# Optimization experiments

Hardware: AMD Instinct MI355X
Metric: run time of the kernel (lower is better)

## Reference

```python
import jax, jax.numpy as jnp
import numpy as np

B, N, IN_DIM = 2, 2048, 1024
DIM, DEPTH, HEADS, DH = 512, 4, 8, 128
INNER = HEADS * DH  # 1024
MLP, NCLS = 1024, 2
EPS = 1e-5


def setup_inputs() -> dict:
    key = jax.random.key(0)
    ks = jax.random.split(key, 10)
    r = lambda k, shape: (jax.random.normal(k, shape, dtype=jnp.float32) * 0.02)
    return {
        "x": jax.random.normal(ks[0], (B, N, IN_DIM), dtype=jnp.float32),
        "mask": jnp.ones((B, N), dtype=jnp.float32),
        "proj_w": r(ks[1], (IN_DIM, DIM)),
        "proj_b": jnp.zeros((DIM,), jnp.float32),
        "cls_token": jax.random.normal(ks[2], (1, 1, DIM), dtype=jnp.float32),
        "ln1_g": jnp.ones((DEPTH, DIM), jnp.float32),
        "ln1_b": jnp.zeros((DEPTH, DIM), jnp.float32),
        "qkv_w": r(ks[3], (DEPTH, DIM, 3 * INNER)),
        "out_w": r(ks[4], (DEPTH, INNER, DIM)),
        "out_b": jnp.zeros((DEPTH, DIM), jnp.float32),
        "ln2_g": jnp.ones((DEPTH, DIM), jnp.float32),
        "ln2_b": jnp.zeros((DEPTH, DIM), jnp.float32),
        "ff_w1": r(ks[5], (DEPTH, DIM, MLP)),
        "ff_b1": jnp.zeros((DEPTH, MLP), jnp.float32),
        "ff_w2": r(ks[6], (DEPTH, MLP, DIM)),
        "ff_b2": jnp.zeros((DEPTH, DIM), jnp.float32),
        "norm_g": jnp.ones((DIM,), jnp.float32),
        "norm_b": jnp.zeros((DIM,), jnp.float32),
        "head_ln_g": jnp.ones((DIM,), jnp.float32),
        "head_ln_b": jnp.zeros((DIM,), jnp.float32),
        "head_w": r(ks[7], (DIM, NCLS)),
        "head_b": jnp.zeros((NCLS,), jnp.float32),
    }


def _ln(x, g, b):
    m = jnp.mean(x, axis=-1, keepdims=True)
    v = jnp.mean((x - m) ** 2, axis=-1, keepdims=True)
    return (x - m) * jax.lax.rsqrt(v + EPS) * g + b


def reference(x, mask, proj_w, proj_b, cls_token, ln1_g, ln1_b, qkv_w, out_w,
              out_b, ln2_g, ln2_b, ff_w1, ff_b1, ff_w2, ff_b2, norm_g, norm_b,
              head_ln_g, head_ln_b, head_w, head_b):
    b = x.shape[0]
    scale = DH ** -0.5
    # input projection + ReLU
    h = jax.nn.relu(x @ proj_w + proj_b)  # [b, n, dim]
    # prepend cls token; extend mask with a 1 for it
    cls = jnp.broadcast_to(cls_token, (b, 1, DIM))
    h = jnp.concatenate([cls, h], axis=1)  # [b, n+1, dim]
    m_full = jnp.concatenate([jnp.ones((b, 1), mask.dtype), mask], axis=1)
    keep = (m_full != 0)[:, None, None, :]  # [b,1,1,n+1]

    for l in range(DEPTH):  # NOTE: original blocks have NO residual connections
        hn = _ln(h, ln1_g[l], ln1_b[l])
        qkv = hn @ qkv_w[l]  # [b, n+1, 3*inner]
        q, k, v = jnp.split(qkv, 3, axis=-1)
        resh = lambda t: t.reshape(b, -1, HEADS, DH).transpose(0, 2, 1, 3)
        q, k, v = resh(q), resh(k), resh(v)  # [b, h, n+1, dh]
        dots = jnp.einsum('bhid,bhjd->bhij', q, k) * scale
        dots = jnp.where(keep, dots, -jnp.inf)
        attn = jax.nn.softmax(dots, axis=-1)
        o = jnp.einsum('bhij,bhjd->bhid', attn, v)
        o = o.transpose(0, 2, 1, 3).reshape(b, -1, INNER)
        h = o @ out_w[l] + out_b[l]  # attention out (no residual)
        hn = _ln(h, ln2_g[l], ln2_b[l])
        h = jax.nn.gelu(hn @ ff_w1[l] + ff_b1[l], approximate=False) @ ff_w2[l] + ff_b2[l]

    pooled = h[:, 0]  # cls pooling
    pooled = _ln(pooled, norm_g, norm_b)
    pooled = _ln(pooled, head_ln_g, head_ln_b)
    return pooled @ head_w + head_b  # [b, num_classes]
```

## Files before the change

kernel.cpp:

```cpp
#include <hip/hip_runtime.h>
#include <hip/hip_bf16.h>
#include <stdint.h>

#define B_      2
#define N_      2048
#define S_      2049
#define SP_     2176
#define MP_     (B_*SP_)
#define IN_DIM_ 1024
#define DIM_    512
#define HEADS_  8
#define DH_     128
#define INNER_  1024
#define MLP_    1024
#define DEPTH_  4
#define NKV_    (SP_/64)
#define NCHUNK_ 3
#define TPC_    12

typedef __bf16 bf16;
typedef __bf16 bf16x4 __attribute__((ext_vector_type(4)));
typedef __bf16 bf16x8 __attribute__((ext_vector_type(8)));
typedef float  f32x4  __attribute__((ext_vector_type(4)));

__device__ __forceinline__ int sw64(int r, int c)  { return r*64  + (c ^ ((r&7)<<3)); }
__device__ __forceinline__ int sw128(int r, int c) { return r*128 + (c ^ ((r&7)<<3)); }
__device__ __forceinline__ int swr64(int r, int c) { return r*64  + (c ^ ((((r&7)^((r>>3)&7)))<<3)); }

__global__ __launch_bounds__(256) void wconv_kernel(const float* __restrict__ src,
                                                    bf16* __restrict__ dst,
                                                    int K, int N)
{
    __shared__ float tile[32][33];
    size_t mo = (size_t)blockIdx.z * K * N;
    int n0 = blockIdx.x * 32, k0 = blockIdx.y * 32;
    int tx = threadIdx.x & 31, ty = threadIdx.x >> 5;
#pragma unroll
    for (int i = 0; i < 32; i += 8)
        tile[ty + i][tx] = src[mo + (size_t)(k0 + ty + i) * N + n0 + tx];
    __syncthreads();
#pragma unroll
    for (int i = 0; i < 32; i += 8)
        dst[mo + (size_t)(n0 + ty + i) * K + k0 + tx] = (bf16)tile[tx][ty + i];
}

__global__ __launch_bounds__(256) void xconv_kernel(const float* __restrict__ x,
                                                    bf16* __restrict__ xb)
{
    int idx = blockIdx.x * 256 + threadIdx.x;
    int row = idx >> 7;
    int c   = (idx & 127) * 8;
    int b = row / SP_, s = row - b * SP_;
    bf16x8 v;
    if (s >= 1 && s <= N_) {
        const float* src = x + (size_t)(b * N_ + s - 1) * IN_DIM_ + c;
#pragma unroll
        for (int i = 0; i < 8; ++i) v[i] = (bf16)src[i];
    } else {
#pragma unroll
        for (int i = 0; i < 8; ++i) v[i] = (bf16)0.f;
    }
    *(bf16x8*)&xb[(size_t)row * IN_DIM_ + c] = v;
}

__global__ __launch_bounds__(256) void mask_kernel(const float* __restrict__ mask,
                                                   float* __restrict__ pb)
{
    int j = blockIdx.x * 256 + threadIdx.x;
    int b = blockIdx.y;
    if (j >= SP_) return;
    float v;
    if (j == 0) v = 0.f;
    else if (j <= N_) v = (mask[(size_t)b * N_ + j - 1] != 0.f) ? 0.f : -1e30f;
    else v = -1e30f;
    pb[(size_t)b * SP_ + j] = v;
}

__global__ void cls_kernel(const float* __restrict__ cls, float* __restrict__ h)
{
    h[(size_t)(blockIdx.x * SP_) * DIM_ + threadIdx.x] = cls[threadIdx.x];
}

__global__ __launch_bounds__(256) void ln_kernel(const float* __restrict__ h,
                                                 const float* __restrict__ g,
                                                 const float* __restrict__ bta,
                                                 bf16* __restrict__ out)
{
    int row  = blockIdx.x * 4 + (threadIdx.x >> 6);
    int lane = threadIdx.x & 63;
    const float* x = h + (size_t)row * DIM_;
    float v[8]; float s = 0.f;
#pragma unroll
    for (int i = 0; i < 8; ++i) { v[i] = x[lane + 64 * i]; s += v[i]; }
#pragma unroll
    for (int o = 32; o; o >>= 1) s += __shfl_xor(s, o);
    float mean = s * (1.f / DIM_);
    float vs = 0.f;
#pragma unroll
    for (int i = 0; i < 8; ++i) { float d = v[i] - mean; vs += d * d; }
#pragma unroll
    for (int o = 32; o; o >>= 1) vs += __shfl_xor(vs, o);
    float rstd = rsqrtf(vs * (1.f / DIM_) + 1e-5f);
    bf16* orow = out + (size_t)row * DIM_;
#pragma unroll
    for (int i = 0; i < 8; ++i)
        orow[lane + 64 * i] = (bf16)((v[i] - mean) * rstd * g[lane + 64 * i] + bta[lane + 64 * i]);
}

template<int BM, int ACT, int OUTBF>
__global__ __launch_bounds__(256) void gemm_bt(const bf16* __restrict__ A,
                                               const bf16* __restrict__ Bt,
                                               const float* __restrict__ bias,
                                               void* __restrict__ Cp,
                                               int M, int N, int K)
{
    constexpr int MF = 4;
    constexpr int NF = (BM == 128) ? 4 : 2;
    __shared__ __align__(16) bf16 As[BM * 64];
    __shared__ __align__(16) bf16 Bs[128 * 64];
    const int tid  = threadIdx.x;
    const int wave = tid >> 6, lane = tid & 63;
    const int bm = blockIdx.x * BM, bn = blockIdx.y * 128;
    const int wr = (BM == 128) ? (wave >> 1) * 64 : 0;
    const int wc = (BM == 128) ? (wave & 1) * 64 : wave * 32;
    const int fr = lane & 15, fk = (lane >> 4) * 8;

    f32x4 acc[MF][NF];
#pragma unroll
    for (int m = 0; m < MF; ++m)
#pragma unroll
        for (int n = 0; n < NF; ++n) acc[m][n] = (f32x4){0.f, 0.f, 0.f, 0.f};

    for (int k0 = 0; k0 < K; k0 += 64) {
#pragma unroll
        for (int t = 0; t < BM / 32; ++t) {
            int e = (t * 256 + tid) * 8;
            int r = e >> 6, c = e & 63;
            *(bf16x8*)&As[sw64(r, c)] = *(const bf16x8*)&A[(size_t)(bm + r) * K + k0 + c];
        }
#pragma unroll
        for (int t = 0; t < 4; ++t) {
            int e = (t * 256 + tid) * 8;
            int r = e >> 6, c = e & 63;
            *(bf16x8*)&Bs[sw64(r, c)] = *(const bf16x8*)&Bt[(size_t)(bn + r) * K + k0 + c];
        }
        __syncthreads();
#pragma unroll
        for (int kk = 0; kk < 2; ++kk) {
            bf16x8 af[MF], bb[NF];
#pragma unroll
            for (int m = 0; m < MF; ++m) af[m] = *(const bf16x8*)&As[sw64(wr + m * 16 + fr, kk * 32 + fk)];
#pragma unroll
            for (int n = 0; n < NF; ++n) bb[n] = *(const bf16x8*)&Bs[sw64(wc + n * 16 + fr, kk * 32 + fk)];
#pragma unroll
            for (int m = 0; m < MF; ++m)
#pragma unroll
                for (int n = 0; n < NF; ++n)
                    acc[m][n] = __builtin_amdgcn_mfma_f32_16x16x32_bf16(af[m], bb[n], acc[m][n], 0, 0, 0);
        }
        __syncthreads();
    }

    const int fc = lane & 15, fr4 = (lane >> 4) * 4;
#pragma unroll
    for (int n = 0; n < NF; ++n) {
        int col = bn + wc + n * 16 + fc;
        float bv = bias ? bias[col] : 0.f;
#pragma unroll
        for (int m = 0; m < MF; ++m) {
#pragma unroll
            for (int j = 0; j < 4; ++j) {
                int row = bm + wr + m * 16 + fr4 + j;
                float v = acc[m][n][j] + bv;
                if (ACT == 1) v = fmaxf(v, 0.f);
                if (ACT == 2) v = 0.5f * v * (1.f + erff(v * 0.70710678118654752f));
                if (OUTBF) ((bf16*)Cp)[(size_t)row * N + col] = (bf16)v;
                else       ((float*)Cp)[(size_t)row * N + col] = v;
            }
        }
    }
}

__global__ __launch_bounds__(256) void attn_kernel(const bf16* __restrict__ qkv,
                                                   const float* __restrict__ pb,
                                                   bf16* __restrict__ o0,
                                                   bf16* __restrict__ o1,
                                                   bf16* __restrict__ o2,
                                                   float* __restrict__ mlbuf)
{
    __shared__ __align__(16) bf16 Ks[64 * 128];
    __shared__ __align__(16) bf16 Vt[128 * 64];
    __shared__ __align__(16) bf16 Ps[4][32 * 64];
    __shared__ float Msk[64];

    const int bh = blockIdx.x, b = bh >> 3, hh = bh & 7;
    const int q0 = blockIdx.y * 128;
    const int chunk = blockIdx.z;
    const int t0 = chunk * TPC_;
    const int t1 = (t0 + TPC_ < NKV_) ? t0 + TPC_ : NKV_;
    bf16* obuf = (chunk == 0) ? o0 : (chunk == 1) ? o1 : o2;

    const int tid = threadIdx.x, wave = tid >> 6, lane = tid & 63;
    const int fc = lane & 15, g = lane >> 4, g8 = g * 8, rr0 = g * 4;

    const bf16* qb = qkv + (size_t)(b * SP_) * (3 * INNER_) + hh * DH_;
    const bf16* kb = qb + INNER_;
    const bf16* vb = qb + 2 * INNER_;

    bf16x8 aq[2][4];
#pragma unroll
    for (int m = 0; m < 2; ++m)
#pragma unroll
        for (int kk = 0; kk < 4; ++kk)
            aq[m][kk] = *(const bf16x8*)&qb[(size_t)(q0 + wave * 32 + m * 16 + fc) * (3 * INNER_) + kk * 32 + g8];

    const int srow = tid >> 4;
    const int scol = (tid & 15) * 8;
    bf16x8 kreg[4], vreg[4];
    float mreg;

    f32x4 accO[2][8];
#pragma unroll
    for (int m = 0; m < 2; ++m)
#pragma unroll
        for (int f = 0; f < 8; ++f) accO[m][f] = (f32x4){0.f, 0.f, 0.f, 0.f};
    float mrow[2] = {-3e38f, -3e38f};
    float lrow[2] = {0.f, 0.f};
    const float scale = 0.08838834764831845f;

    auto issue = [&](int kt) {
        int j0 = kt * 64;
#pragma unroll
        for (int t = 0; t < 4; ++t) {
            kreg[t] = *(const bf16x8*)&kb[(size_t)(j0 + t * 16 + srow) * (3 * INNER_) + scol];
            vreg[t] = *(const bf16x8*)&vb[(size_t)(j0 + t * 16 + srow) * (3 * INNER_) + scol];
        }
        mreg = pb[(size_t)b * SP_ + j0 + (tid & 63)];
    };

    issue(t0);
    for (int kt = t0; kt < t1; ++kt) {
        __syncthreads();
        {
#pragma unroll
            for (int t = 0; t < 4; ++t) {
                *(bf16x8*)&Ks[sw128(t * 16 + srow, scol)] = kreg[t];
#pragma unroll
                for (int i = 0; i < 8; ++i) Vt[swr64(scol + i, t * 16 + srow)] = vreg[t][i];
            }
            if (tid < 64) Msk[tid] = mreg;
        }
        __syncthreads();
        if (kt + 1 < t1) issue(kt + 1);

        f32x4 sf[2][4];
#pragma unroll
        for (int m = 0; m < 2; ++m)
#pragma unroll
            for (int f = 0; f < 4; ++f) sf[m][f] = (f32x4){0.f, 0.f, 0.f, 0.f};
        __builtin_amdgcn_s_setprio(1);
#pragma unroll
        for (int kk = 0; kk < 4; ++kk) {
            bf16x8 bk[4];
#pragma unroll
            for (int f = 0; f < 4; ++f) bk[f] = *(const bf16x8*)&Ks[sw128(f * 16 + fc, kk * 32 + g8)];
#pragma unroll
            for (int m = 0; m < 2; ++m)
#pragma unroll
                for (int f = 0; f < 4; ++f)
                    sf[m][f] = __builtin_amdgcn_mfma_f32_16x16x32_bf16(bk[f], aq[m][kk], sf[m][f], 0, 0, 0);
        }
        __builtin_amdgcn_s_setprio(0);

        float rmax[2] = {-3e38f, -3e38f};
#pragma unroll
        for (int f = 0; f < 4; ++f) {
            f32x4 mb = *(const f32x4*)&Msk[f * 16 + rr0];
#pragma unroll
            for (int m = 0; m < 2; ++m)
#pragma unroll
                for (int r = 0; r < 4; ++r) {
                    float s = sf[m][f][r] * scale + mb[r];
                    sf[m][f][r] = s;
                    rmax[m] = fmaxf(rmax[m], s);
                }
        }
        float corr[2];
#pragma unroll
        for (int m = 0; m < 2; ++m) {
            rmax[m] = fmaxf(rmax[m], __shfl_xor(rmax[m], 16));
            rmax[m] = fmaxf(rmax[m], __shfl_xor(rmax[m], 32));
            float mn = fmaxf(mrow[m], rmax[m]);
            corr[m] = __expf(mrow[m] - mn);
            mrow[m] = mn;
            lrow[m] *= corr[m];
        }
#pragma unroll
        for (int m = 0; m < 2; ++m)
#pragma unroll
            for (int f = 0; f < 4; ++f) {
                bf16x4 pw;
#pragma unroll
                for (int r = 0; r < 4; ++r) {
                    float p = __expf(sf[m][f][r] - mrow[m]);
                    lrow[m] += p;
                    pw[r] = (bf16)p;
                }
                *(bf16x4*)&Ps[wave][swr64(m * 16 + fc, f * 16 + rr0)] = pw;
            }
#pragma unroll
        for (int m = 0; m < 2; ++m) {
            float c0 = __shfl(corr[m], rr0 + 0);
            float c1 = __shfl(corr[m], rr0 + 1);
            float c2 = __shfl(corr[m], rr0 + 2);
            float c3 = __shfl(corr[m], rr0 + 3);
#pragma unroll
            for (int f = 0; f < 8; ++f) {
                accO[m][f][0] *= c0; accO[m][f][1] *= c1;
                accO[m][f][2] *= c2; accO[m][f][3] *= c3;
            }
        }
        __builtin_amdgcn_s_setprio(1);
#pragma unroll
        for (int kk = 0; kk < 2; ++kk) {
            bf16x8 ap[2];
#pragma unroll
            for (int m = 0; m < 2; ++m) ap[m] = *(const bf16x8*)&Ps[wave][swr64(m * 16 + fc, kk * 32 + g8)];
#pragma unroll
            for (int f = 0; f < 8; ++f) {
                bf16x8 bv = *(const bf16x8*)&Vt[swr64(f * 16 + fc, kk * 32 + g8)];
#pragma unroll
                for (int m = 0; m < 2; ++m)
                    accO[m][f] = __builtin_amdgcn_mfma_f32_16x16x32_bf16(ap[m], bv, accO[m][f], 0, 0, 0);
            }
        }
        __builtin_amdgcn_s_setprio(0);
    }

#pragma unroll
    for (int m = 0; m < 2; ++m) {
        float l = lrow[m];
        l += __shfl_xor(l, 16);
        l += __shfl_xor(l, 32);
        if (g == 0) {
            int q = q0 + wave * 32 + m * 16 + fc;
            size_t mi = ((size_t)(chunk * B_ * HEADS_ + bh) * SP_ + q) * 2;
            mlbuf[mi + 0] = mrow[m];
            mlbuf[mi + 1] = l;
        }
        float linv = (l > 0.f) ? 1.f / l : 0.f;
        float l0 = __shfl(linv, rr0 + 0);
        float l1 = __shfl(linv, rr0 + 1);
        float l2 = __shfl(linv, rr0 + 2);
        float l3 = __shfl(linv, rr0 + 3);
#pragma unroll
        for (int f = 0; f < 8; ++f) {
            int col = hh * DH_ + f * 16 + fc;
            size_t base = (size_t)(b * SP_ + q0 + wave * 32 + m * 16 + rr0) * INNER_ + col;
            obuf[base + 0 * INNER_] = (bf16)(accO[m][f][0] * l0);
            obuf[base + 1 * INNER_] = (bf16)(accO[m][f][1] * l1);
            obuf[base + 2 * INNER_] = (bf16)(accO[m][f][2] * l2);
            obuf[base + 3 * INNER_] = (bf16)(accO[m][f][3] * l3);
        }
    }
}

__global__ __launch_bounds__(256) void attn_combine_kernel(const bf16* __restrict__ o0,
                                                           const bf16* __restrict__ o1,
                                                           bf16* __restrict__ o2,
                                                           const float* __restrict__ mlbuf)
{
    const int bh = blockIdx.y, b = bh >> 3, hh = bh & 7;
    int gx = blockIdx.x * 256 + threadIdx.x;
    int q  = gx >> 4;
    int d  = (gx & 15) * 8;

    float m0, l0v, m1, l1v, m2, l2v;
    {
        size_t mi0 = ((size_t)(0 * B_ * HEADS_ + bh) * SP_ + q) * 2;
        size_t mi1 = ((size_t)(1 * B_ * HEADS_ + bh) * SP_ + q) * 2;
        size_t mi2 = ((size_t)(2 * B_ * HEADS_ + bh) * SP_ + q) * 2;
        m0 = mlbuf[mi0]; l0v = mlbuf[mi0 + 1];
        m1 = mlbuf[mi1]; l1v = mlbuf[mi1 + 1];
        m2 = mlbuf[mi2]; l2v = mlbuf[mi2 + 1];
    }
    float M = fmaxf(fmaxf(m0, m1), m2);
    float w0 = l0v * __expf(m0 - M);
    float w1 = l1v * __expf(m1 - M);
    float w2 = l2v * __expf(m2 - M);
    float den = w0 + w1 + w2;
    float r = (den > 0.f) ? 1.f / den : 0.f;
    w0 *= r; w1 *= r; w2 *= r;

    size_t base = (size_t)(b * SP_ + q) * INNER_ + hh * DH_ + d;
    bf16x8 v0 = *(const bf16x8*)&o0[base];
    bf16x8 v1 = *(const bf16x8*)&o1[base];
    bf16x8 v2 = *(const bf16x8*)&o2[base];
    bf16x8 out;
#pragma unroll
    for (int i = 0; i < 8; ++i)
        out[i] = (bf16)(w0 * (float)v0[i] + w1 * (float)v1[i] + w2 * (float)v2[i]);
    *(bf16x8*)&o2[base] = out;
}

__global__ __launch_bounds__(64) void head_kernel(const float* __restrict__ h,
                                                  const float* __restrict__ ng, const float* __restrict__ nb,
                                                  const float* __restrict__ hg, const float* __restrict__ hb,
                                                  const float* __restrict__ hw, const float* __restrict__ hbi,
                                                  float* __restrict__ out)
{
    int b = blockIdx.x, lane = threadIdx.x;
    const float* xr = h + (size_t)(b * SP_) * DIM_;
    float v[8]; float s = 0.f;
#pragma unroll
    for (int i = 0; i < 8; ++i) { v[i] = xr[lane + 64 * i]; s += v[i]; }
#pragma unroll
    for (int o = 32; o; o >>= 1) s += __shfl_xor(s, o);
    float mean = s * (1.f / DIM_); float vs = 0.f;
#pragma unroll
    for (int i = 0; i < 8; ++i) { float d = v[i] - mean; vs += d * d; }
#pragma unroll
    for (int o = 32; o; o >>= 1) vs += __shfl_xor(vs, o);
    float rstd = rsqrtf(vs * (1.f / DIM_) + 1e-5f);
#pragma unroll
    for (int i = 0; i < 8; ++i) v[i] = (v[i] - mean) * rstd * ng[lane + 64 * i] + nb[lane + 64 * i];
    s = 0.f;
#pragma unroll
    for (int i = 0; i < 8; ++i) s += v[i];
#pragma unroll
    for (int o = 32; o; o >>= 1) s += __shfl_xor(s, o);
    mean = s * (1.f / DIM_); vs = 0.f;
#pragma unroll
    for (int i = 0; i < 8; ++i) { float d = v[i] - mean; vs += d * d; }
#pragma unroll
    for (int o = 32; o; o >>= 1) vs += __shfl_xor(vs, o);
    rstd = rsqrtf(vs * (1.f / DIM_) + 1e-5f);
#pragma unroll
    for (int i = 0; i < 8; ++i) v[i] = (v[i] - mean) * rstd * hg[lane + 64 * i] + hb[lane + 64 * i];
    float a0 = 0.f, a1 = 0.f;
#pragma unroll
    for (int i = 0; i < 8; ++i) {
        a0 += v[i] * hw[(lane + 64 * i) * 2 + 0];
        a1 += v[i] * hw[(lane + 64 * i) * 2 + 1];
    }
#pragma unroll
    for (int o = 32; o; o >>= 1) { a0 += __shfl_xor(a0, o); a1 += __shfl_xor(a1, o); }
    if (lane == 0) { out[b * 2 + 0] = a0 + hbi[0]; out[b * 2 + 1] = a1 + hbi[1]; }
}

extern "C" void kernel_launch(void* const* d_in, const int* in_sizes, int n_in,
                              void* d_out, int out_size, void* d_ws, size_t ws_size,
                              hipStream_t stream)
{
    const float* x       = (const float*)d_in[0];
    const float* mask    = (const float*)d_in[1];
    const float* proj_w  = (const float*)d_in[2];
    const float* proj_b  = (const float*)d_in[3];
    const float* cls_tok = (const float*)d_in[4];
    const float* ln1_g   = (const float*)d_in[5];
    const float* ln1_b   = (const float*)d_in[6];
    const float* qkv_w   = (const float*)d_in[7];
    const float* out_w   = (const float*)d_in[8];
    const float* out_b   = (const float*)d_in[9];
    const float* ln2_g   = (const float*)d_in[10];
    const float* ln2_b   = (const float*)d_in[11];
    const float* ff_w1   = (const float*)d_in[12];
    const float* ff_b1   = (const float*)d_in[13];
    const float* ff_w2   = (const float*)d_in[14];
    const float* ff_b2   = (const float*)d_in[15];
    const float* norm_g  = (const float*)d_in[16];
    const float* norm_b  = (const float*)d_in[17];
    const float* hln_g   = (const float*)d_in[18];
    const float* hln_b   = (const float*)d_in[19];
    const float* head_w  = (const float*)d_in[20];
    const float* head_b  = (const float*)d_in[21];

    char* p = (char*)d_ws;
    auto alloc = [&](size_t bytes) { char* r = p; p += (bytes + 255) & ~(size_t)255; return r; };
    bf16*  x_bf    = (bf16*)alloc((size_t)MP_ * IN_DIM_ * 2);
    float* h       = (float*)alloc((size_t)MP_ * DIM_ * 4);
    bf16*  hn_bf   = (bf16*)alloc((size_t)MP_ * DIM_ * 2);
    bf16*  qkv_bf  = (bf16*)alloc((size_t)MP_ * 3 * INNER_ * 2);
    bf16*  o_bf    = (bf16*)alloc((size_t)MP_ * INNER_ * 2);
    bf16*  ff1_bf  = (bf16*)alloc((size_t)MP_ * MLP_ * 2);
    bf16*  proj_wt = (bf16*)alloc((size_t)DIM_ * IN_DIM_ * 2);
    bf16*  qkv_wt  = (bf16*)alloc((size_t)DEPTH_ * 3 * INNER_ * DIM_ * 2);
    bf16*  out_wt  = (bf16*)alloc((size_t)DEPTH_ * DIM_ * INNER_ * 2);
    bf16*  ff1_wt  = (bf16*)alloc((size_t)DEPTH_ * MLP_ * DIM_ * 2);
    bf16*  ff2_wt  = (bf16*)alloc((size_t)DEPTH_ * DIM_ * MLP_ * 2);
    float* pbias   = (float*)alloc((size_t)B_ * SP_ * 4);
    if ((size_t)(p - (char*)d_ws) > ws_size) return;
    float* mlbuf = (float*)hn_bf;

    wconv_kernel<<<dim3(DIM_ / 32, IN_DIM_ / 32, 1), 256, 0, stream>>>(proj_w, proj_wt, IN_DIM_, DIM_);
    wconv_kernel<<<dim3(3 * INNER_ / 32, DIM_ / 32, DEPTH_), 256, 0, stream>>>(qkv_w, qkv_wt, DIM_, 3 * INNER_);
    wconv_kernel<<<dim3(DIM_ / 32, INNER_ / 32, DEPTH_), 256, 0, stream>>>(out_w, out_wt, INNER_, DIM_);
    wconv_kernel<<<dim3(MLP_ / 32, DIM_ / 32, DEPTH_), 256, 0, stream>>>(ff_w1, ff1_wt, DIM_, MLP_);
    wconv_kernel<<<dim3(DIM_ / 32, MLP_ / 32, DEPTH_), 256, 0, stream>>>(ff_w2, ff2_wt, MLP_, DIM_);

    xconv_kernel<<<MP_ * IN_DIM_ / 8 / 256, 256, 0, stream>>>(x, x_bf);
    mask_kernel<<<dim3((SP_ + 255) / 256, B_), 256, 0, stream>>>(mask, pbias);

    gemm_bt<64, 1, 0><<<dim3(MP_ / 64, DIM_ / 128), 256, 0, stream>>>(x_bf, proj_wt, proj_b, h, MP_, DIM_, IN_DIM_);
    cls_kernel<<<B_, DIM_, 0, stream>>>(cls_tok, h);

    for (int l = 0; l < DEPTH_; ++l) {
        ln_kernel<<<MP_ / 4, 256, 0, stream>>>(h, ln1_g + l * DIM_, ln1_b + l * DIM_, hn_bf);
        gemm_bt<128, 0, 1><<<dim3(MP_ / 128, 3 * INNER_ / 128), 256, 0, stream>>>(
            hn_bf, qkv_wt + (size_t)l * 3 * INNER_ * DIM_, nullptr, qkv_bf, MP_, 3 * INNER_, DIM_);
        attn_kernel<<<dim3(B_ * HEADS_, SP_ / 128, NCHUNK_), 256, 0, stream>>>(
            qkv_bf, pbias, x_bf, ff1_bf, o_bf, mlbuf);
        attn_combine_kernel<<<dim3(SP_ * 16 / 256, B_ * HEADS_), 256, 0, stream>>>(
            x_bf, ff1_bf, o_bf, mlbuf);
        gemm_bt<64, 0, 0><<<dim3(MP_ / 64, DIM_ / 128), 256, 0, stream>>>(
            o_bf, out_wt + (size_t)l * DIM_ * INNER_, out_b + l * DIM_, h, MP_, DIM_, INNER_);
        ln_kernel<<<MP_ / 4, 256, 0, stream>>>(h, ln2_g + l * DIM_, ln2_b + l * DIM_, hn_bf);
        gemm_bt<64, 2, 1><<<dim3(MP_ / 64, MLP_ / 128), 256, 0, stream>>>(
            hn_bf, ff1_wt + (size_t)l * MLP_ * DIM_, ff_b1 + l * MLP_, ff1_bf, MP_, MLP_, DIM_);
        gemm_bt<64, 0, 0><<<dim3(MP_ / 64, DIM_ / 128), 256, 0, stream>>>(
            ff1_bf, ff2_wt + (size_t)l * DIM_ * MLP_, ff_b2 + l * DIM_, h, MP_, DIM_, MLP_);
    }

    head_kernel<<<B_, 64, 0, stream>>>(h, norm_g, norm_b, hln_g, hln_b, head_w, head_b, (float*)d_out);
}
```

Measured before the change: 862.3 us.

## Prefetch GEMM tiles to registers, add 64x64 tiles, four attention chunks, lazy rescale

The GEMM now loads the next K-tile into registers while the current tile is consumed, and drops one barrier per iteration. It also gains a BN template parameter so the narrow N=512 GEMMs run with 64x64 tiles and get more blocks. Attention splits the KV range into four chunks instead of three and reuses the K shared buffer for P to save LDS. Online-softmax rescaling is skipped unless the row max grows by more than a threshold. The combine step handles four partials, using the h buffer as scratch for the extra one, which relies on h being dead at that point.

```diff
diff --git a/kernel.cpp b/kernel.cpp
--- a/kernel.cpp
+++ b/kernel.cpp
@@ -15,8 +15,8 @@
 #define MLP_    1024
 #define DEPTH_  4
 #define NKV_    (SP_/64)
-#define NCHUNK_ 3
-#define TPC_    12
+#define NCHUNK_ 4
+#define TPC_    9
 
 typedef __bf16 bf16;
 typedef __bf16 bf16x4 __attribute__((ext_vector_type(4)));
@@ -107,22 +107,23 @@
         orow[lane + 64 * i] = (bf16)((v[i] - mean) * rstd * g[lane + 64 * i] + bta[lane + 64 * i]);
 }
 
-template<int BM, int ACT, int OUTBF>
+template<int BM, int BN, int ACT, int OUTBF>
 __global__ __launch_bounds__(256) void gemm_bt(const bf16* __restrict__ A,
                                                const bf16* __restrict__ Bt,
                                                const float* __restrict__ bias,
                                                void* __restrict__ Cp,
                                                int M, int N, int K)
 {
-    constexpr int MF = 4;
+    constexpr int MF = (BM == 128) ? 4 : ((BN == 128) ? 4 : 2);
     constexpr int NF = (BM == 128) ? 4 : 2;
+    constexpr int AT = BM / 32, BT = BN / 32;
     __shared__ __align__(16) bf16 As[BM * 64];
-    __shared__ __align__(16) bf16 Bs[128 * 64];
+    __shared__ __align__(16) bf16 Bs[BN * 64];
     const int tid  = threadIdx.x;
     const int wave = tid >> 6, lane = tid & 63;
-    const int bm = blockIdx.x * BM, bn = blockIdx.y * 128;
-    const int wr = (BM == 128) ? (wave >> 1) * 64 : 0;
-    const int wc = (BM == 128) ? (wave & 1) * 64 : wave * 32;
+    const int bm = blockIdx.x * BM, bn = blockIdx.y * BN;
+    const int wr = (BM == 128) ? (wave >> 1) * 64 : ((BN == 64) ? (wave >> 1) * 32 : 0);
+    const int wc = (BM == 128) ? (wave & 1) * 64 : ((BN == 64) ? (wave & 1) * 32 : wave * 32);
     const int fr = lane & 15, fk = (lane >> 4) * 8;
 
     f32x4 acc[MF][NF];
@@ -131,20 +132,35 @@
 #pragma unroll
         for (int n = 0; n < NF; ++n) acc[m][n] = (f32x4){0.f, 0.f, 0.f, 0.f};
 
+    bf16x8 apre[AT], bpre[BT];
+    auto ldg = [&](int k0) {
+#pragma unroll
+        for (int t = 0; t < AT; ++t) {
+            int e = (t * 256 + tid) * 8;
+            apre[t] = *(const bf16x8*)&A[(size_t)(bm + (e >> 6)) * K + k0 + (e & 63)];
+        }
+#pragma unroll
+        for (int t = 0; t < BT; ++t) {
+            int e = (t * 256 + tid) * 8;
+            bpre[t] = *(const bf16x8*)&Bt[(size_t)(bn + (e >> 6)) * K + k0 + (e & 63)];
+        }
+    };
+
+    ldg(0);
     for (int k0 = 0; k0 < K; k0 += 64) {
-#pragma unroll
-        for (int t = 0; t < BM / 32; ++t) {
+        __syncthreads();
+#pragma unroll
+        for (int t = 0; t < AT; ++t) {
             int e = (t * 256 + tid) * 8;
-            int r = e >> 6, c = e & 63;
-            *(bf16x8*)&As[sw64(r, c)] = *(const bf16x8*)&A[(size_t)(bm + r) * K + k0 + c];
-        }
-#pragma unroll
-        for (int t = 0; t < 4; ++t) {
+            *(bf16x8*)&As[sw64(e >> 6, e & 63)] = apre[t];
+        }
+#pragma unroll
+        for (int t = 0; t < BT; ++t) {
             int e = (t * 256 + tid) * 8;
-            int r = e >> 6, c = e & 63;
-            *(bf16x8*)&Bs[sw64(r, c)] = *(const bf16x8*)&Bt[(size_t)(bn + r) * K + k0 + c];
+            *(bf16x8*)&Bs[sw64(e >> 6, e & 63)] = bpre[t];
         }
         __syncthreads();
+        if (k0 + 64 < K) ldg(k0 + 64);
 #pragma unroll
         for (int kk = 0; kk < 2; ++kk) {
             bf16x8 af[MF], bb[NF];
@@ -158,7 +174,6 @@
                 for (int n = 0; n < NF; ++n)
                     acc[m][n] = __builtin_amdgcn_mfma_f32_16x16x32_bf16(af[m], bb[n], acc[m][n], 0, 0, 0);
         }
-        __syncthreads();
     }
 
     const int fc = lane & 15, fr4 = (lane >> 4) * 4;
@@ -186,11 +201,11 @@
                                                    bf16* __restrict__ o0,
                                                    bf16* __restrict__ o1,
                                                    bf16* __restrict__ o2,
+                                                   bf16* __restrict__ o3,
                                                    float* __restrict__ mlbuf)
 {
-    __shared__ __align__(16) bf16 Ks[64 * 128];
+    __shared__ __align__(16) bf16 KsPs[64 * 128];
     __shared__ __align__(16) bf16 Vt[128 * 64];
-    __shared__ __align__(16) bf16 Ps[4][32 * 64];
     __shared__ float Msk[64];
 
     const int bh = blockIdx.x, b = bh >> 3, hh = bh & 7;
@@ -198,10 +213,11 @@
     const int chunk = blockIdx.z;
     const int t0 = chunk * TPC_;
     const int t1 = (t0 + TPC_ < NKV_) ? t0 + TPC_ : NKV_;
-    bf16* obuf = (chunk == 0) ? o0 : (chunk == 1) ? o1 : o2;
+    bf16* obuf = (chunk == 0) ? o0 : (chunk == 1) ? o1 : (chunk == 2) ? o2 : o3;
 
     const int tid = threadIdx.x, wave = tid >> 6, lane = tid & 63;
     const int fc = lane & 15, g = lane >> 4, g8 = g * 8, rr0 = g * 4;
+    bf16* Pw = &KsPs[wave * 2048];
 
     const bf16* qb = qkv + (size_t)(b * SP_) * (3 * INNER_) + hh * DH_;
     const bf16* kb = qb + INNER_;
@@ -244,7 +260,7 @@
         {
 #pragma unroll
             for (int t = 0; t < 4; ++t) {
-                *(bf16x8*)&Ks[sw128(t * 16 + srow, scol)] = kreg[t];
+                *(bf16x8*)&KsPs[sw128(t * 16 + srow, scol)] = kreg[t];
 #pragma unroll
                 for (int i = 0; i < 8; ++i) Vt[swr64(scol + i, t * 16 + srow)] = vreg[t][i];
             }
@@ -263,7 +279,7 @@
         for (int kk = 0; kk < 4; ++kk) {
             bf16x8 bk[4];
 #pragma unroll
-            for (int f = 0; f < 4; ++f) bk[f] = *(const bf16x8*)&Ks[sw128(f * 16 + fc, kk * 32 + g8)];
+            for (int f = 0; f < 4; ++f) bk[f] = *(const bf16x8*)&KsPs[sw128(f * 16 + fc, kk * 32 + g8)];
 #pragma unroll
             for (int m = 0; m < 2; ++m)
 #pragma unroll
@@ -285,47 +301,51 @@
                     rmax[m] = fmaxf(rmax[m], s);
                 }
         }
-        float corr[2];
 #pragma unroll
         for (int m = 0; m < 2; ++m) {
             rmax[m] = fmaxf(rmax[m], __shfl_xor(rmax[m], 16));
             rmax[m] = fmaxf(rmax[m], __shfl_xor(rmax[m], 32));
-            float mn = fmaxf(mrow[m], rmax[m]);
-            corr[m] = __expf(mrow[m] - mn);
-            mrow[m] = mn;
-            lrow[m] *= corr[m];
-        }
+            if (__any(rmax[m] > mrow[m] + 5.f)) {
+                float mn = fmaxf(mrow[m], rmax[m]);
+                float corr = __expf(mrow[m] - mn);
+                mrow[m] = mn;
+                lrow[m] *= corr;
+                float c0 = __shfl(corr, rr0 + 0);
+                float c1 = __shfl(corr, rr0 + 1);
+                float c2 = __shfl(corr, rr0 + 2);
+                float c3 = __shfl(corr, rr0 + 3);
+#pragma unroll
+                for (int f = 0; f < 8; ++f) {
+                    accO[m][f][0] *= c0; accO[m][f][1] *= c1;
+                    accO[m][f][2] *= c2; accO[m][f][3] *= c3;
+                }
+            }
+        }
+        bf16x4 pw[2][4];
 #pragma unroll
         for (int m = 0; m < 2; ++m)
 #pragma unroll
             for (int f = 0; f < 4; ++f) {
-                bf16x4 pw;
 #pragma unroll
                 for (int r = 0; r < 4; ++r) {
                     float p = __expf(sf[m][f][r] - mrow[m]);
                     lrow[m] += p;
-                    pw[r] = (bf16)p;
+                    pw[m][f][r] = (bf16)p;
                 }
-                *(bf16x4*)&Ps[wave][swr64(m * 16 + fc, f * 16 + rr0)] = pw;
             }
-#pragma unroll
-        for (int m = 0; m < 2; ++m) {
-            float c0 = __shfl(corr[m], rr0 + 0);
-            float c1 = __shfl(corr[m], rr0 + 1);
-            float c2 = __shfl(corr[m], rr0 + 2);
-            float c3 = __shfl(corr[m], rr0 + 3);
-#pragma unroll
-            for (int f = 0; f < 8; ++f) {
-                accO[m][f][0] *= c0; accO[m][f][1] *= c1;
-                accO[m][f][2] *= c2; accO[m][f][3] *= c3;
-            }
-        }
+        __syncthreads();
+#pragma unroll
+        for (int m = 0; m < 2; ++m)
+#pragma unroll
+            for (int f = 0; f < 4; ++f)
+                *(bf16x4*)&Pw[swr64(m * 16 + fc, f * 16 + rr0)] = pw[m][f];
+
         __builtin_amdgcn_s_setprio(1);
 #pragma unroll
         for (int kk = 0; kk < 2; ++kk) {
             bf16x8 ap[2];
 #pragma unroll
-            for (int m = 0; m < 2; ++m) ap[m] = *(const bf16x8*)&Ps[wave][swr64(m * 16 + fc, kk * 32 + g8)];
+            for (int m = 0; m < 2; ++m) ap[m] = *(const bf16x8*)&Pw[swr64(m * 16 + fc, kk * 32 + g8)];
 #pragma unroll
             for (int f = 0; f < 8; ++f) {
                 bf16x8 bv = *(const bf16x8*)&Vt[swr64(f * 16 + fc, kk * 32 + g8)];
@@ -367,7 +387,8 @@
 
 __global__ __launch_bounds__(256) void attn_combine_kernel(const bf16* __restrict__ o0,
                                                            const bf16* __restrict__ o1,
-                                                           bf16* __restrict__ o2,
+                                                           const bf16* __restrict__ o2,
+                                                           bf16* __restrict__ o3,
                                                            const float* __restrict__ mlbuf)
 {
     const int bh = blockIdx.y, b = bh >> 3, hh = bh & 7;
@@ -375,32 +396,32 @@
     int q  = gx >> 4;
     int d  = (gx & 15) * 8;
 
-    float m0, l0v, m1, l1v, m2, l2v;
-    {
-        size_t mi0 = ((size_t)(0 * B_ * HEADS_ + bh) * SP_ + q) * 2;
-        size_t mi1 = ((size_t)(1 * B_ * HEADS_ + bh) * SP_ + q) * 2;
-        size_t mi2 = ((size_t)(2 * B_ * HEADS_ + bh) * SP_ + q) * 2;
-        m0 = mlbuf[mi0]; l0v = mlbuf[mi0 + 1];
-        m1 = mlbuf[mi1]; l1v = mlbuf[mi1 + 1];
-        m2 = mlbuf[mi2]; l2v = mlbuf[mi2 + 1];
-    }
-    float M = fmaxf(fmaxf(m0, m1), m2);
-    float w0 = l0v * __expf(m0 - M);
-    float w1 = l1v * __expf(m1 - M);
-    float w2 = l2v * __expf(m2 - M);
-    float den = w0 + w1 + w2;
+    float mv[NCHUNK_], lv[NCHUNK_];
+#pragma unroll
+    for (int c = 0; c < NCHUNK_; ++c) {
+        size_t mi = ((size_t)(c * B_ * HEADS_ + bh) * SP_ + q) * 2;
+        mv[c] = mlbuf[mi];
+        lv[c] = mlbuf[mi + 1];
+    }
+    float M = mv[0];
+#pragma unroll
+    for (int c = 1; c < NCHUNK_; ++c) M = fmaxf(M, mv[c]);
+    float w[NCHUNK_], den = 0.f;
+#pragma unroll
+    for (int c = 0; c < NCHUNK_; ++c) { w[c] = lv[c] * __expf(mv[c] - M); den += w[c]; }
     float r = (den > 0.f) ? 1.f / den : 0.f;
-    w0 *= r; w1 *= r; w2 *= r;
 
     size_t base = (size_t)(b * SP_ + q) * INNER_ + hh * DH_ + d;
     bf16x8 v0 = *(const bf16x8*)&o0[base];
     bf16x8 v1 = *(const bf16x8*)&o1[base];
     bf16x8 v2 = *(const bf16x8*)&o2[base];
+    bf16x8 v3 = *(const bf16x8*)&o3[base];
     bf16x8 out;
 #pragma unroll
     for (int i = 0; i < 8; ++i)
-        out[i] = (bf16)(w0 * (float)v0[i] + w1 * (float)v1[i] + w2 * (float)v2[i]);
-    *(bf16x8*)&o2[base] = out;
+        out[i] = (bf16)((w[0] * (float)v0[i] + w[1] * (float)v1[i]
+                       + w[2] * (float)v2[i] + w[3] * (float)v3[i]) * r);
+    *(bf16x8*)&o3[base] = out;
 }
 
 __global__ __launch_bounds__(64) void head_kernel(const float* __restrict__ h,
@@ -501,23 +522,23 @@
     xconv_kernel<<<MP_ * IN_DIM_ / 8 / 256, 256, 0, stream>>>(x, x_bf);
     mask_kernel<<<dim3((SP_ + 255) / 256, B_), 256, 0, stream>>>(mask, pbias);
 
-    gemm_bt<64, 1, 0><<<dim3(MP_ / 64, DIM_ / 128), 256, 0, stream>>>(x_bf, proj_wt, proj_b, h, MP_, DIM_, IN_DIM_);
+    gemm_bt<64, 64, 1, 0><<<dim3(MP_ / 64, DIM_ / 64), 256, 0, stream>>>(x_bf, proj_wt, proj_b, h, MP_, DIM_, IN_DIM_);
     cls_kernel<<<B_, DIM_, 0, stream>>>(cls_tok, h);
 
     for (int l = 0; l < DEPTH_; ++l) {
         ln_kernel<<<MP_ / 4, 256, 0, stream>>>(h, ln1_g + l * DIM_, ln1_b + l * DIM_, hn_bf);
-        gemm_bt<128, 0, 1><<<dim3(MP_ / 128, 3 * INNER_ / 128), 256, 0, stream>>>(
+        gemm_bt<128, 128, 0, 1><<<dim3(MP_ / 128, 3 * INNER_ / 128), 256, 0, stream>>>(
             hn_bf, qkv_wt + (size_t)l * 3 * INNER_ * DIM_, nullptr, qkv_bf, MP_, 3 * INNER_, DIM_);
         attn_kernel<<<dim3(B_ * HEADS_, SP_ / 128, NCHUNK_), 256, 0, stream>>>(
-            qkv_bf, pbias, x_bf, ff1_bf, o_bf, mlbuf);
+            qkv_bf, pbias, x_bf, ff1_bf, (bf16*)h, o_bf, mlbuf);
         attn_combine_kernel<<<dim3(SP_ * 16 / 256, B_ * HEADS_), 256, 0, stream>>>(
-            x_bf, ff1_bf, o_bf, mlbuf);
-        gemm_bt<64, 0, 0><<<dim3(MP_ / 64, DIM_ / 128), 256, 0, stream>>>(
+            x_bf, ff1_bf, (const bf16*)h, o_bf, mlbuf);
+        gemm_bt<64, 64, 0, 0><<<dim3(MP_ / 64, DIM_ / 64), 256, 0, stream>>>(
             o_bf, out_wt + (size_t)l * DIM_ * INNER_, out_b + l * DIM_, h, MP_, DIM_, INNER_);
         ln_kernel<<<MP_ / 4, 256, 0, stream>>>(h, ln2_g + l * DIM_, ln2_b + l * DIM_, hn_bf);
-        gemm_bt<64, 2, 1><<<dim3(MP_ / 64, MLP_ / 128), 256, 0, stream>>>(
+        gemm_bt<64, 128, 2, 1><<<dim3(MP_ / 64, MLP_ / 128), 256, 0, stream>>>(
             hn_bf, ff1_wt + (size_t)l * MLP_ * DIM_, ff_b1 + l * MLP_, ff1_bf, MP_, MLP_, DIM_);
-        gemm_bt<64, 0, 0><<<dim3(MP_ / 64, DIM_ / 128), 256, 0, stream>>>(
+        gemm_bt<64, 64, 0, 0><<<dim3(MP_ / 64, DIM_ / 64), 256, 0, stream>>>(
             ff1_bf, ff2_wt + (size_t)l * DIM_ * MLP_, ff_b2 + l * DIM_, h, MP_, DIM_, MLP_);
     }
 
```

New measurement: 816.7 us. 5.3% less time.
